# Kernel optimization log

Measured on AMD Instinct MI355X. Metric: run time of the kernel, lower is better.

The kernel has to match this reference:

```python
import jax, jax.numpy as jnp
import numpy as np

N_NODES = 50000


def _gcn_norm(edge_index, num_nodes):
    # PyG gcn_norm with add_self_loops=True, edge_weight=1
    src = jnp.concatenate([edge_index[0], jnp.arange(num_nodes, dtype=edge_index.dtype)])
    dst = jnp.concatenate([edge_index[1], jnp.arange(num_nodes, dtype=edge_index.dtype)])
    deg = jax.ops.segment_sum(jnp.ones_like(dst, dtype=jnp.float32), dst,
                              num_segments=num_nodes)
    deg_inv_sqrt = jnp.where(deg > 0, jax.lax.rsqrt(deg), 0.0)
    norm = deg_inv_sqrt[src] * deg_inv_sqrt[dst]  # [E + N]
    return src, dst, norm


def _gcn_conv(x, src, dst, norm, W, b, num_nodes):
    h = x @ W                                   # [N, F_out] linear first
    msg = h[src] * norm[:, None]                # gather + scale  [E+N, F_out]
    out = jax.ops.segment_sum(msg, dst, num_segments=num_nodes)  # scatter-add
    return out + b


def setup_inputs() -> dict:
    key = jax.random.key(0)
    k1, k2, k3, k4 = jax.random.split(key, 4)
    IN_C, HID, OUT_C, E = 128, 96, 48, 800000
    x = jax.random.normal(k1, (N_NODES, IN_C), dtype=jnp.float32)
    edge_index = jax.random.randint(k2, (2, E), 0, N_NODES, dtype=jnp.int64)
    # Glorot-style scaled weights
    W1 = jax.random.normal(k3, (IN_C, HID), dtype=jnp.float32) * (1.0 / np.sqrt(IN_C))
    b1 = jnp.zeros((HID,), dtype=jnp.float32)
    W2 = jax.random.normal(k4, (HID, OUT_C), dtype=jnp.float32) * (1.0 / np.sqrt(HID))
    b2 = jnp.zeros((OUT_C,), dtype=jnp.float32)
    return {"x": x, "edge_index": edge_index, "W1": W1, "b1": b1, "W2": W2, "b2": b2}


def reference(x, edge_index, W1, b1, W2, b2):
    # cached=True: normalization computed once and reused by both layers
    src, dst, norm = _gcn_norm(edge_index, N_NODES)
    h = jax.nn.relu(_gcn_conv(x, src, dst, norm, W1, b1, N_NODES))
    return _gcn_conv(h, src, dst, norm, W2, b2, N_NODES)
```

## Files before the change

kernel.cpp:

```cpp
#include <hip/hip_runtime.h>

static constexpr int IN_C  = 128;
static constexpr int HID   = 96;
static constexpr int OUT_C = 48;

static constexpr int NPART     = 8;
static constexpr int FILL_ITER = 16;
static constexpr int CHUNK     = 256 * FILL_ITER;

typedef short bf16x8 __attribute__((ext_vector_type(8)));
typedef float f32x4  __attribute__((ext_vector_type(4)));


__device__ __forceinline__ unsigned short f2bf(float f) {
  union { float f; unsigned u; } c; c.f = f;
  unsigned r = c.u + 0x7fffu + ((c.u >> 16) & 1u);
  return (unsigned short)(r >> 16);
}
__device__ __forceinline__ float bflo(unsigned u) {
  union { unsigned u; float f; } c; c.u = u << 16; return c.f;
}
__device__ __forceinline__ float bfhi(unsigned u) {
  union { unsigned u; float f; } c; c.u = u & 0xffff0000u; return c.f;
}

__device__ __forceinline__ void wprep_one(const float* W, uint4* Wt,
                                          int K, int M, int idx) {
  int lane = idx & 63;
  int t = idx >> 6;
  int KB = K / 32;
  int c  = t / KB;
  int kb = t - c * KB;
  int col = c * 16 + (lane & 15);
  int k0  = kb * 32 + (lane >> 4) * 8;
  unsigned pk[4];
#pragma unroll
  for (int q = 0; q < 4; ++q) {
    unsigned lo = f2bf(W[(size_t)(k0 + 2 * q) * M + col]);
    unsigned hi = f2bf(W[(size_t)(k0 + 2 * q + 1) * M + col]);
    pk[q] = lo | (hi << 16);
  }
  Wt[idx] = make_uint4(pk[0], pk[1], pk[2], pk[3]);
}

__global__ void k_init(int* __restrict__ cnt, int n, int nbN,
                       const float* __restrict__ W1, uint4* __restrict__ Wt1, int T1,
                       const float* __restrict__ W2, uint4* __restrict__ Wt2, int T2) {
  int b = blockIdx.x;
  if (b < nbN) {
    int i = b * 256 + threadIdx.x;
    if (i < n) cnt[i] = 0;
  } else {
    int idx = (b - nbN) * 256 + threadIdx.x;
    if (idx < T1) wprep_one(W1, Wt1, IN_C, HID, idx);
    else if (idx < T1 + T2) wprep_one(W2, Wt2, HID, OUT_C, idx - T1);
  }
}


__global__ void k_count(const int* __restrict__ dst, int* __restrict__ cnt,
                        int* __restrict__ perm, int E) {
  int e = blockIdx.x * blockDim.x + threadIdx.x;
  if (e < E) perm[e] = atomicAdd(&cnt[dst[e]], 1);
}

__global__ void k_scan_block(const int* __restrict__ in, int* __restrict__ out_excl,
                             int* __restrict__ bsum, int n) {
  __shared__ int sm[256];
  int i = blockIdx.x * 256 + threadIdx.x;
  int v = (i < n) ? in[i] : 0;
  int val = v;
  sm[threadIdx.x] = val;
  __syncthreads();
  for (int off = 1; off < 256; off <<= 1) {
    int t = (threadIdx.x >= (unsigned)off) ? sm[threadIdx.x - off] : 0;
    __syncthreads();
    val += t;
    sm[threadIdx.x] = val;
    __syncthreads();
  }
  if (i < n) out_excl[i] = val - v;
  if (threadIdx.x == 255) bsum[blockIdx.x] = val;
}

__global__ void k_finish(int* __restrict__ rs, const int* __restrict__ boff,
                         const int* __restrict__ cnt,
                         float* __restrict__ dinv, int n) {
  int i = blockIdx.x * 256 + threadIdx.x;
  if (i >= n) return;
  rs[i] = rs[i] + boff[blockIdx.x];
  dinv[i] = rsqrtf((float)cnt[i] + 1.0f);
}

__global__ __launch_bounds__(256) void k_fill_part(
    const int* __restrict__ src, const int* __restrict__ dst,
    const int* __restrict__ perm, const int* __restrict__ rs,
    int* __restrict__ csr, int E, int P) {
  int lo = blockIdx.x * P;
  int hi = lo + P;
  int base = blockIdx.y * CHUNK + threadIdx.x;
#pragma unroll
  for (int i = 0; i < FILL_ITER; ++i) {
    int e = base + i * 256;
    if (e < E) {
      int d = dst[e];
      if (d >= lo && d < hi) {
        csr[rs[d] + perm[e]] = src[e];
      }
    }
  }
}


template <int K, int M, bool ABF16>
__global__ __launch_bounds__(256) void k_gemm(const void* __restrict__ Xv,
                                              const uint4* __restrict__ Wt,
                                              const float* __restrict__ dinv,
                                              unsigned short* __restrict__ Y,
                                              int N) {
  constexpr int KB = K / 32;
  constexpr int CT = M / 16;
  constexpr int GR = K / 8;
  __shared__ unsigned short lds[64 * 128];
  const int tid  = threadIdx.x;
  const int base = blockIdx.x * 64;

  for (int idx = tid; idx < 64 * GR; idx += 256) {
    int row = idx / GR;
    int g   = idx - row * GR;
    int srow = min(base + row, N - 1);
    uint4 pk;
    if (ABF16) {
      pk = *(const uint4*)((const unsigned short*)Xv + (size_t)srow * K + g * 8);
    } else {
      const float* xp = (const float*)Xv + (size_t)srow * K + g * 8;
      float4 v0 = *(const float4*)xp;
      float4 v1 = *(const float4*)(xp + 4);
      pk.x = (unsigned)f2bf(v0.x) | ((unsigned)f2bf(v0.y) << 16);
      pk.y = (unsigned)f2bf(v0.z) | ((unsigned)f2bf(v0.w) << 16);
      pk.z = (unsigned)f2bf(v1.x) | ((unsigned)f2bf(v1.y) << 16);
      pk.w = (unsigned)f2bf(v1.z) | ((unsigned)f2bf(v1.w) << 16);
    }
    int gs = g ^ (row & 7);
    *(uint4*)(&lds[row * 128 + gs * 8]) = pk;
  }
  __syncthreads();

  const int lane = tid & 63;
  const int wv   = tid >> 6;
  const int lrow = wv * 16 + (lane & 15);
  const int khi  = lane >> 4;

  f32x4 acc[CT];
#pragma unroll
  for (int c = 0; c < CT; ++c) acc[c] = (f32x4){0.f, 0.f, 0.f, 0.f};

  const bf16x8* Wb = (const bf16x8*)Wt;
#pragma unroll
  for (int kb = 0; kb < KB; ++kb) {
    int j  = khi + kb * 4;
    int js = j ^ (lrow & 7);
    bf16x8 a = *(const bf16x8*)(&lds[lrow * 128 + js * 8]);
#pragma unroll
    for (int c = 0; c < CT; ++c) {
      bf16x8 b = Wb[(c * KB + kb) * 64 + lane];
      acc[c] = __builtin_amdgcn_mfma_f32_16x16x32_bf16(a, b, acc[c], 0, 0, 0);
    }
  }

  const int r0 = base + wv * 16 + khi * 4;
#pragma unroll
  for (int i = 0; i < 4; ++i) {
    int row = r0 + i;
    if (row < N) {
      float d = dinv[row];
      unsigned short* yp = Y + (size_t)row * M + (lane & 15);
#pragma unroll
      for (int c = 0; c < CT; ++c) {
        yp[c * 16] = f2bf(acc[c][i] * d);
      }
    }
  }
}


__device__ __forceinline__ void bfacc(float* a, const uint4& v) {
  a[0] += bflo(v.x); a[1] += bfhi(v.x);
  a[2] += bflo(v.y); a[3] += bfhi(v.y);
  a[4] += bflo(v.z); a[5] += bfhi(v.z);
  a[6] += bflo(v.w); a[7] += bfhi(v.w);
}

template <int M, bool RELU, bool OBF16>
__global__ __launch_bounds__(256) void k_agg(const unsigned short* __restrict__ Hs,
                                             const int* __restrict__ csr,
                                             const int* __restrict__ rs,
                                             const int* __restrict__ cnt,
                                             const float* __restrict__ dinv,
                                             const float* __restrict__ bias,
                                             void* __restrict__ outv, int N) {
  constexpr int JC = M / 8;
  int gid = blockIdx.x * blockDim.x + threadIdx.x;
  int n = gid / JC;
  if (n >= N) return;
  int f8 = (gid - n * JC) * 8;
  float dn = dinv[n];
  float a[8] = {};
  {
    uint4 sv = *(const uint4*)(Hs + (size_t)n * M + f8);
    bfacc(a, sv);
  }
  int p = rs[n];
  int e = cnt[n];
  int i = 0;
  for (; i + 8 <= e; i += 8) {
    int s0 = csr[p + i];
    int s1 = csr[p + i + 1];
    int s2 = csr[p + i + 2];
    int s3 = csr[p + i + 3];
    int s4 = csr[p + i + 4];
    int s5 = csr[p + i + 5];
    int s6 = csr[p + i + 6];
    int s7 = csr[p + i + 7];
    uint4 g0 = *(const uint4*)(Hs + (size_t)s0 * M + f8);
    uint4 g1 = *(const uint4*)(Hs + (size_t)s1 * M + f8);
    uint4 g2 = *(const uint4*)(Hs + (size_t)s2 * M + f8);
    uint4 g3 = *(const uint4*)(Hs + (size_t)s3 * M + f8);
    uint4 g4 = *(const uint4*)(Hs + (size_t)s4 * M + f8);
    uint4 g5 = *(const uint4*)(Hs + (size_t)s5 * M + f8);
    uint4 g6 = *(const uint4*)(Hs + (size_t)s6 * M + f8);
    uint4 g7 = *(const uint4*)(Hs + (size_t)s7 * M + f8);
    bfacc(a, g0); bfacc(a, g1); bfacc(a, g2); bfacc(a, g3);
    bfacc(a, g4); bfacc(a, g5); bfacc(a, g6); bfacc(a, g7);
  }
  for (; i + 4 <= e; i += 4) {
    int s0 = csr[p + i];
    int s1 = csr[p + i + 1];
    int s2 = csr[p + i + 2];
    int s3 = csr[p + i + 3];
    uint4 g0 = *(const uint4*)(Hs + (size_t)s0 * M + f8);
    uint4 g1 = *(const uint4*)(Hs + (size_t)s1 * M + f8);
    uint4 g2 = *(const uint4*)(Hs + (size_t)s2 * M + f8);
    uint4 g3 = *(const uint4*)(Hs + (size_t)s3 * M + f8);
    bfacc(a, g0); bfacc(a, g1); bfacc(a, g2); bfacc(a, g3);
  }
  for (; i < e; ++i) {
    int s = csr[p + i];
    uint4 g = *(const uint4*)(Hs + (size_t)s * M + f8);
    bfacc(a, g);
  }
  float r[8];
#pragma unroll
  for (int q = 0; q < 8; ++q) {
    r[q] = fmaf(dn, a[q], bias[f8 + q]);
    if (RELU) r[q] = fmaxf(r[q], 0.0f);
  }
  if (OBF16) {
    uint4 pk;
    pk.x = (unsigned)f2bf(r[0]) | ((unsigned)f2bf(r[1]) << 16);
    pk.y = (unsigned)f2bf(r[2]) | ((unsigned)f2bf(r[3]) << 16);
    pk.z = (unsigned)f2bf(r[4]) | ((unsigned)f2bf(r[5]) << 16);
    pk.w = (unsigned)f2bf(r[6]) | ((unsigned)f2bf(r[7]) << 16);
    *(uint4*)((unsigned short*)outv + (size_t)n * M + f8) = pk;
  } else {
    float* op = (float*)outv + (size_t)n * M + f8;
    *(float4*)(op)     = make_float4(r[0], r[1], r[2], r[3]);
    *(float4*)(op + 4) = make_float4(r[4], r[5], r[6], r[7]);
  }
}


extern "C" void kernel_launch(void* const* d_in, const int* in_sizes, int n_in,
                              void* d_out, int out_size, void* d_ws, size_t ws_size,
                              hipStream_t stream) {
  const float* x  = (const float*)d_in[0];
  const int*   ei = (const int*)d_in[1];
  const float* W1 = (const float*)d_in[2];
  const float* b1 = (const float*)d_in[3];
  const float* W2 = (const float*)d_in[4];
  const float* b2 = (const float*)d_in[5];
  float* out = (float*)d_out;

  const int N = in_sizes[0] / IN_C;
  const int E = in_sizes[1] / 2;
  const int* src = ei;
  const int* dst = ei + E;

  char* ws = (char*)d_ws;
  size_t off = 0;
  auto alloc = [&](size_t bytes) -> void* {
    void* p = ws + off;
    off = (off + bytes + 255) & ~(size_t)255;
    return p;
  };
  int*   cnt    = (int*)alloc((size_t)N * 4);
  int*   rs     = (int*)alloc((size_t)N * 4);
  float* dinv   = (float*)alloc((size_t)N * 4);
  int*   bsum   = (int*)alloc(256 * 4);
  int*   boff   = (int*)alloc(256 * 4);
  int*   junk   = (int*)alloc(256 * 4);
  int*   perm   = (int*)alloc((size_t)E * 4);
  int*   csr    = (int*)alloc((size_t)E * 4);
  unsigned short* hbf = (unsigned short*)alloc((size_t)N * HID * 2);
  unsigned short* hb2 = (unsigned short*)alloc((size_t)N * HID * 2);
  constexpr int T1 = (HID / 16) * (IN_C / 32) * 64;
  constexpr int T2 = (OUT_C / 16) * (HID / 32) * 64;
  uint4* Wt1 = (uint4*)alloc((size_t)T1 * 16);
  uint4* Wt2 = (uint4*)alloc((size_t)T2 * 16);

  const int nbN = (N + 255) / 256;
  const int nbE = (E + 255) / 256;
  const int P   = (N + NPART - 1) / NPART;
  const int wprepBlocks = (T1 + T2 + 255) / 256;

  k_init<<<nbN + wprepBlocks, 256, 0, stream>>>(cnt, N, nbN, W1, Wt1, T1, W2, Wt2, T2);
  k_count<<<nbE, 256, 0, stream>>>(dst, cnt, perm, E);
  k_scan_block<<<nbN, 256, 0, stream>>>(cnt, rs, bsum, N);
  k_scan_block<<<1, 256, 0, stream>>>(bsum, boff, junk, nbN);
  k_finish<<<nbN, 256, 0, stream>>>(rs, boff, cnt, dinv, N);
  dim3 fg(NPART, (E + CHUNK - 1) / CHUNK);
  k_fill_part<<<fg, 256, 0, stream>>>(src, dst, perm, rs, csr, E, P);

  const int rowBlocks = (N + 63) / 64;

  {
    k_gemm<IN_C, HID, false><<<rowBlocks, 256, 0, stream>>>(x, Wt1, dinv, hbf, N);
    int t = N * (HID / 8);
    k_agg<HID, true, true><<<(t + 255) / 256, 256, 0, stream>>>(hbf, csr, rs, cnt, dinv, b1, hb2, N);
  }
  {
    k_gemm<HID, OUT_C, true><<<rowBlocks, 256, 0, stream>>>(hb2, Wt2, dinv, hbf, N);
    int t = N * (OUT_C / 8);
    k_agg<OUT_C, false, false><<<(t + 255) / 256, 256, 0, stream>>>(hbf, csr, rs, cnt, dinv, b2, out, N);
  }
}
```

Baseline: 128.1 us.

## Fold block-offset scan into finish kernel and co-launch CSR fill with first GEMM

Drops the single-block scan launch: each finish block now reduces the preceding block sums in shared memory to get its own offset. The CSR fill blocks and the layer-1 GEMM blocks are merged into one launch that branches on block index, so the two independent jobs run side by side. This removes two kernel launches and their serialization gaps. In exchange, fill blocks now reserve the GEMM's shared memory, which can lower their occupancy, and every finish block repeats a small reduction.

```diff
diff --git a/kernel.cpp b/kernel.cpp
--- a/kernel.cpp
+++ b/kernel.cpp
@@ -83,47 +83,40 @@
   if (threadIdx.x == 255) bsum[blockIdx.x] = val;
 }
 
-__global__ void k_finish(int* __restrict__ rs, const int* __restrict__ boff,
+__global__ void k_finish(int* __restrict__ rs, const int* __restrict__ bsum,
                          const int* __restrict__ cnt,
                          float* __restrict__ dinv, int n) {
-  int i = blockIdx.x * 256 + threadIdx.x;
-  if (i >= n) return;
-  rs[i] = rs[i] + boff[blockIdx.x];
-  dinv[i] = rsqrtf((float)cnt[i] + 1.0f);
-}
-
-__global__ __launch_bounds__(256) void k_fill_part(
-    const int* __restrict__ src, const int* __restrict__ dst,
-    const int* __restrict__ perm, const int* __restrict__ rs,
-    int* __restrict__ csr, int E, int P) {
-  int lo = blockIdx.x * P;
-  int hi = lo + P;
-  int base = blockIdx.y * CHUNK + threadIdx.x;
-#pragma unroll
-  for (int i = 0; i < FILL_ITER; ++i) {
-    int e = base + i * 256;
-    if (e < E) {
-      int d = dst[e];
-      if (d >= lo && d < hi) {
-        csr[rs[d] + perm[e]] = src[e];
-      }
-    }
+  __shared__ int sm[256];
+  int b = blockIdx.x;
+  int t = threadIdx.x;
+  int v = (t < b) ? bsum[t] : 0;
+  sm[t] = v;
+  __syncthreads();
+#pragma unroll
+  for (int off = 128; off > 0; off >>= 1) {
+    if (t < off) sm[t] += sm[t + off];
+    __syncthreads();
+  }
+  int boff = sm[0];
+  int i = b * 256 + t;
+  if (i < n) {
+    rs[i] = rs[i] + boff;
+    dinv[i] = rsqrtf((float)cnt[i] + 1.0f);
   }
 }
 
 
 template <int K, int M, bool ABF16>
-__global__ __launch_bounds__(256) void k_gemm(const void* __restrict__ Xv,
-                                              const uint4* __restrict__ Wt,
-                                              const float* __restrict__ dinv,
-                                              unsigned short* __restrict__ Y,
-                                              int N) {
+__device__ __forceinline__ void gemm_body(const void* __restrict__ Xv,
+                                          const uint4* __restrict__ Wt,
+                                          const float* __restrict__ dinv,
+                                          unsigned short* __restrict__ Y,
+                                          int N, int gb, unsigned short* lds,
+                                          int tid) {
   constexpr int KB = K / 32;
   constexpr int CT = M / 16;
   constexpr int GR = K / 8;
-  __shared__ unsigned short lds[64 * 128];
-  const int tid  = threadIdx.x;
-  const int base = blockIdx.x * 64;
+  const int base = gb * 64;
 
   for (int idx = tid; idx < 64 * GR; idx += 256) {
     int row = idx / GR;
@@ -181,6 +174,43 @@
       }
     }
   }
+}
+
+__global__ __launch_bounds__(256) void k_fill_gemm1(
+    const int* __restrict__ src, const int* __restrict__ dst,
+    const int* __restrict__ perm, const int* __restrict__ rs,
+    int* __restrict__ csr, int E, int P, int fillBlocks,
+    const float* __restrict__ X, const uint4* __restrict__ Wt,
+    const float* __restrict__ dinv, unsigned short* __restrict__ Y, int N) {
+  __shared__ unsigned short lds[64 * 128];
+  int bid = blockIdx.x;
+  if (bid < fillBlocks) {
+    int lo = (bid & (NPART - 1)) * P;
+    int hi = lo + P;
+    int base = (bid >> 3) * CHUNK + threadIdx.x;
+#pragma unroll
+    for (int i = 0; i < FILL_ITER; ++i) {
+      int e = base + i * 256;
+      if (e < E) {
+        int d = dst[e];
+        if (d >= lo && d < hi) {
+          csr[rs[d] + perm[e]] = src[e];
+        }
+      }
+    }
+    return;
+  }
+  gemm_body<IN_C, HID, false>(X, Wt, dinv, Y, N, bid - fillBlocks, lds, threadIdx.x);
+}
+
+template <int K, int M, bool ABF16>
+__global__ __launch_bounds__(256) void k_gemm(const void* __restrict__ Xv,
+                                              const uint4* __restrict__ Wt,
+                                              const float* __restrict__ dinv,
+                                              unsigned short* __restrict__ Y,
+                                              int N) {
+  __shared__ unsigned short lds[64 * 128];
+  gemm_body<K, M, ABF16>(Xv, Wt, dinv, Y, N, blockIdx.x, lds, threadIdx.x);
 }
 
 
@@ -297,8 +327,6 @@
   int*   rs     = (int*)alloc((size_t)N * 4);
   float* dinv   = (float*)alloc((size_t)N * 4);
   int*   bsum   = (int*)alloc(256 * 4);
-  int*   boff   = (int*)alloc(256 * 4);
-  int*   junk   = (int*)alloc(256 * 4);
   int*   perm   = (int*)alloc((size_t)E * 4);
   int*   csr    = (int*)alloc((size_t)E * 4);
   unsigned short* hbf = (unsigned short*)alloc((size_t)N * HID * 2);
@@ -312,19 +340,18 @@
   const int nbE = (E + 255) / 256;
   const int P   = (N + NPART - 1) / NPART;
   const int wprepBlocks = (T1 + T2 + 255) / 256;
+  const int fillBlocks  = NPART * ((E + CHUNK - 1) / CHUNK);
+  const int rowBlocks   = (N + 63) / 64;
 
   k_init<<<nbN + wprepBlocks, 256, 0, stream>>>(cnt, N, nbN, W1, Wt1, T1, W2, Wt2, T2);
   k_count<<<nbE, 256, 0, stream>>>(dst, cnt, perm, E);
   k_scan_block<<<nbN, 256, 0, stream>>>(cnt, rs, bsum, N);
-  k_scan_block<<<1, 256, 0, stream>>>(bsum, boff, junk, nbN);
-  k_finish<<<nbN, 256, 0, stream>>>(rs, boff, cnt, dinv, N);
-  dim3 fg(NPART, (E + CHUNK - 1) / CHUNK);
-  k_fill_part<<<fg, 256, 0, stream>>>(src, dst, perm, rs, csr, E, P);
-
-  const int rowBlocks = (N + 63) / 64;
+  k_finish<<<nbN, 256, 0, stream>>>(rs, bsum, cnt, dinv, N);
+
+  k_fill_gemm1<<<fillBlocks + rowBlocks, 256, 0, stream>>>(
+      src, dst, perm, rs, csr, E, P, fillBlocks, x, Wt1, dinv, hbf, N);
 
   {
-    k_gemm<IN_C, HID, false><<<rowBlocks, 256, 0, stream>>>(x, Wt1, dinv, hbf, N);
     int t = N * (HID / 8);
     k_agg<HID, true, true><<<(t + 255) / 256, 256, 0, stream>>>(hbf, csr, rs, cnt, dinv, b1, hb2, N);
   }
```

Result: no change. 128.0 us (-0.1%).
